# Optimization experiments

Hardware: AMD Instinct MI355X
Metric: run time of the kernel (lower is better)

Reference implementation:

```python
import jax, jax.numpy as jnp
import numpy as np
from jax import lax

H, N, L = 256, 64, 4096
DT_MIN, DT_MAX = 0.001, 0.1


def make_hippo(n_state):
    n = jnp.arange(n_state)
    P = jnp.sqrt(1.0 + 2.0 * n)
    A = P[:, None] * P[None, :]
    A = jnp.tril(A) - jnp.diag(n.astype(jnp.float32))
    B = jnp.sqrt(2.0 * n + 1.0)[:, None]
    return -A, B


def setup_inputs() -> dict:
    key = jax.random.key(0)
    A, B = make_hippo(N)
    A = jnp.broadcast_to(A, (H, N, N))            # H N N
    B = jnp.broadcast_to(B, (H, N, 1))            # H N 1
    log_dt = jnp.linspace(DT_MIN, DT_MAX, H)      # note: used directly as dt (as in source)
    u = jax.random.normal(key, (L,), dtype=jnp.float32)
    return {"u": u, "A": A, "B": B, "log_dt": log_dt}


def reference(u, A, B, log_dt):
    dt = log_dt  # `.dt` property returns log_dt.value unchanged
    I = jnp.eye(N, dtype=A.dtype)
    dt2A = (dt[:, None, None] * 0.5) * A                      # H N N
    BL = jnp.linalg.inv(I - dt2A)                             # H N N (batched inv)
    Ab = BL @ (I + dt2A)                                      # H N N
    Bb = (BL * dt[:, None, None]) @ B                         # H N 1

    # Bb * u broadcast: L H N
    Bb_u = u[:, None, None] * Bb[None, :, :, 0]

    def step(x, b_k):
        x1 = jnp.einsum('hnm,hm->hn', Ab, x) + b_k            # H N
        return x1, x1

    state0 = jnp.zeros((H, N), dtype=u.dtype)
    _, x = lax.scan(step, state0, Bb_u)                       # x: L H N
    return x
```

## Files before the change

### kernel.cpp

```cpp
#include <hip/hip_runtime.h>

#define NHEAD 256

typedef _Float16 f16x8 __attribute__((ext_vector_type(8)));
typedef float f32x4 __attribute__((ext_vector_type(4)));

__device__ __forceinline__ int mel(int r, int c) {
  return (r << 6) + ((((c >> 3) ^ r) & 7) << 3) + (c & 7);
}
__device__ __forceinline__ f16x8 ldfrag(const _Float16* M, int r, int u) {
  return *(const f16x8*)(M + (r << 6) + (((u ^ r) & 7) << 3));
}
__device__ __forceinline__ f32x4 MF(f16x8 a, f16x8 b, f32x4 c) {
  return __builtin_amdgcn_mfma_f32_16x16x32_f16(a, b, c, 0, 0, 0);
}

__device__ __forceinline__ void mmstep8(const _Float16* A, const _Float16* BT,
                                        _Float16* Dr, _Float16* Dt, int dr0,
                                        int nrb, int limit, int w, int c15,
                                        int g) {
  const int wc = w & 3;
  f16x8 b0 = ldfrag(BT, (wc << 4) + c15, g);
  f16x8 b1 = ldfrag(BT, (wc << 4) + c15, 4 + g);
  for (int ib = (w >> 2); ib < nrb; ib += 2) {
    f32x4 acc = {0.f, 0.f, 0.f, 0.f};
    f16x8 a0 = ldfrag(A, (ib << 4) + c15, g);
    f16x8 a1 = ldfrag(A, (ib << 4) + c15, 4 + g);
    acc = MF(a0, b0, acc);
    acc = MF(a1, b1, acc);
#pragma unroll
    for (int j = 0; j < 4; ++j) {
      const int lr = (ib << 4) + (g << 2) + j;
      if (lr < limit) {
        const int rr = dr0 + lr;
        const int cc = (wc << 4) + c15;
        const _Float16 v = (_Float16)acc[j];
        Dr[mel(rr, cc)] = v;
        Dt[mel(cc, rr)] = v;
      }
    }
  }
}

__global__ __launch_bounds__(512, 2) void hippo_fused(
    const float* __restrict__ u, const float* __restrict__ Ag,
    const float* __restrict__ Bv, const float* __restrict__ dtv,
    float* __restrict__ out) {
  const int h = blockIdx.x;
  const int t = threadIdx.x;
  const int w = t >> 6;
  const int lane = t & 63;
  const int c15 = lane & 15;
  const int g = lane >> 4;

  __shared__ __align__(16) _Float16 URV[4 * 4616];
  __shared__ __align__(16) _Float16 RING[4 * 4096];
  __shared__ __align__(16) char UNI[49152];
  __shared__ __align__(16) _Float16 PB23[2 * 4096];
  __shared__ float RED[8][64];
  __shared__ float KC[64];

  float* Ms = (float*)UNI;
  float* Xs = (float*)(UNI + 16384);
  float* invd = (float*)(UNI + 16384 + 17408);
  _Float16* PB0 = (_Float16*)UNI;
  _Float16* PB1 = PB0 + 4096;
  _Float16* PB4 = (_Float16*)(UNI + 16384);
  _Float16* PB5 = PB4 + 4096;
  _Float16* PB2 = PB23;
  _Float16* PB3 = PB23 + 4096;

  for (int s = 0; s < 4; ++s)
    for (int x = t; x < 4616; x += 512) {
      const int q = 4095 - x - s;
      URV[s * 4616 + x] = (q >= 0) ? (_Float16)u[q] : (_Float16)0.f;
    }
  const float dt = dtv[h];
  const float* Ah = Ag + (size_t)h * 4096;
  for (int idx = t; idx < 4096; idx += 512) {
    const int r = idx >> 6, c = idx & 63;
    const float a = Ah[idx];
    const float half_ = 0.5f * dt * a;
    const float id = (r == c) ? 1.0f : 0.0f;
    Ms[r * 64 + c] = id - half_;
    Xs[r * 68 + c] = id + half_;
  }
  if (t < 64) {
    Xs[t * 68 + 64] = dt * Bv[h * 64 + t];
    Xs[t * 68 + 65] = 0.f;
    Xs[t * 68 + 66] = 0.f;
    Xs[t * 68 + 67] = 0.f;
    invd[t] = 1.0f / (1.0f - 0.5f * dt * Ah[t * 65]);
  }
  __syncthreads();

  for (int k = 0; k < 64; k += 4) {
    if (t < 68) {
      const int c = t;
      const float x0 = Xs[k * 68 + c] * invd[k];
      const float x1 = (Xs[(k + 1) * 68 + c] - Ms[(k + 1) * 64 + k] * x0) * invd[k + 1];
      const float x2 = (Xs[(k + 2) * 68 + c] - Ms[(k + 2) * 64 + k] * x0 -
                        Ms[(k + 2) * 64 + k + 1] * x1) * invd[k + 2];
      const float x3 = (Xs[(k + 3) * 68 + c] - Ms[(k + 3) * 64 + k] * x0 -
                        Ms[(k + 3) * 64 + k + 1] * x1 -
                        Ms[(k + 3) * 64 + k + 2] * x2) * invd[k + 3];
      Xs[k * 68 + c] = x0;
      Xs[(k + 1) * 68 + c] = x1;
      Xs[(k + 2) * 68 + c] = x2;
      Xs[(k + 3) * 68 + c] = x3;
    }
    __syncthreads();
    const int nwork = (60 - k) * 17;
    for (int idx = t; idx < nwork; idx += 512) {
      const int r = k + 4 + idx / 17;
      const int cu = (idx % 17) * 4;
      float4 xr = *(float4*)&Xs[r * 68 + cu];
      const float m0 = Ms[r * 64 + k], m1 = Ms[r * 64 + k + 1];
      const float m2 = Ms[r * 64 + k + 2], m3 = Ms[r * 64 + k + 3];
      const float4 a0 = *(float4*)&Xs[k * 68 + cu];
      const float4 a1 = *(float4*)&Xs[(k + 1) * 68 + cu];
      const float4 a2 = *(float4*)&Xs[(k + 2) * 68 + cu];
      const float4 a3 = *(float4*)&Xs[(k + 3) * 68 + cu];
      xr.x -= m0 * a0.x + m1 * a1.x + m2 * a2.x + m3 * a3.x;
      xr.y -= m0 * a0.y + m1 * a1.y + m2 * a2.y + m3 * a3.y;
      xr.z -= m0 * a0.z + m1 * a1.z + m2 * a2.z + m3 * a3.z;
      xr.w -= m0 * a0.w + m1 * a1.w + m2 * a2.w + m3 * a3.w;
      *(float4*)&Xs[r * 68 + cu] = xr;
    }
    __syncthreads();
  }

  for (int idx = t; idx < 4096; idx += 512) {
    const int r = idx >> 6, cc = idx & 63;
    const _Float16 v = (_Float16)Xs[r * 68 + cc];
    PB0[mel(r, cc)] = v;
    PB1[mel(cc, r)] = v;
  }
  if (t < 64) {
    const float bb = Xs[t * 68 + 64];
    KC[t] = bb;
    PB2[mel(0, t)] = (_Float16)bb;
    PB3[mel(t, 0)] = (_Float16)bb;
  }
  __syncthreads();

  {
    const int mrow = t & 63;
    const float4* ar = (const float4*)(Xs + mrow * 68 + w * 8);
    const float4 av0 = ar[0], av1 = ar[1];
    const int jb = w * 8;
    RED[w][mrow] = av0.x * KC[jb] + av0.y * KC[jb + 1] + av0.z * KC[jb + 2] +
                   av0.w * KC[jb + 3] + av1.x * KC[jb + 4] + av1.y * KC[jb + 5] +
                   av1.z * KC[jb + 6] + av1.w * KC[jb + 7];
    __syncthreads();
    if (t < 64) {
      float s2 = 0.f;
#pragma unroll
      for (int qq = 0; qq < 8; ++qq) s2 += RED[qq][t];
      PB2[mel(1, t)] = (_Float16)s2;
      PB3[mel(t, 1)] = (_Float16)s2;
    }
    __syncthreads();
  }

  mmstep8(PB0, PB1, PB4, PB5, 0, 4, 64, w, c15, g); __syncthreads();
  mmstep8(PB2, PB4, PB2, PB3, 2, 1, 2, w, c15, g);  __syncthreads();
  mmstep8(PB4, PB5, PB0, PB1, 0, 4, 64, w, c15, g); __syncthreads();
  mmstep8(PB2, PB0, PB2, PB3, 4, 1, 4, w, c15, g);  __syncthreads();
  mmstep8(PB0, PB1, PB4, PB5, 0, 4, 64, w, c15, g); __syncthreads();
  mmstep8(PB2, PB4, PB2, PB3, 8, 1, 8, w, c15, g);  __syncthreads();
  mmstep8(PB4, PB5, PB0, PB1, 0, 4, 64, w, c15, g); __syncthreads();
  mmstep8(PB2, PB0, PB2, PB3, 16, 1, 16, w, c15, g); __syncthreads();
  mmstep8(PB0, PB1, PB4, PB5, 0, 4, 64, w, c15, g); __syncthreads();
  mmstep8(PB2, PB4, PB2, PB3, 32, 2, 32, w, c15, g); __syncthreads();
  mmstep8(PB4, PB5, PB0, PB1, 0, 4, 64, w, c15, g); __syncthreads();

  f16x8 bt[8][4];
  f16x8 bc[2][4];
  auto LB = [&](f16x8* dst, const _Float16* BT, int kk) {
#pragma unroll
    for (int nb = 0; nb < 4; ++nb)
      dst[nb] = ldfrag(BT, (nb << 4) + c15, (kk << 2) + g);
  };

  LB(bt[0], PB3, 0); LB(bt[1], PB3, 1);
  mmstep8(PB2, PB0, PB4, PB5, 0, 4, 64, w, c15, g); __syncthreads();
  LB(bt[2], PB5, 0); LB(bt[3], PB5, 1);
  mmstep8(PB4, PB0, PB2, PB3, 0, 4, 64, w, c15, g); __syncthreads();
  LB(bt[4], PB3, 0); LB(bt[5], PB3, 1);
  mmstep8(PB2, PB0, PB4, PB5, 0, 4, 64, w, c15, g); __syncthreads();
  LB(bt[6], PB5, 0); LB(bt[7], PB5, 1);
  mmstep8(PB1, PB0, PB2, PB3, 0, 4, 64, w, c15, g); __syncthreads();
  mmstep8(PB2, PB3, PB4, PB1, 0, 4, 64, w, c15, g); __syncthreads();
  LB(bc[0], PB1, 0); LB(bc[1], PB1, 1);
  __syncthreads();

  const int chain = w & 3;
  const int half = w >> 2;
  _Float16* ringw = RING + (chain << 12);
  float* outh = out + (h << 6);
  const int lanebase = (g << 3) - c15;

#pragma unroll 1
  for (int mstep = 0; mstep < 16; ++mstep) {
    const int c = chain + (mstep << 2);
    f32x4 acc[2][4];
#pragma unroll
    for (int ibl = 0; ibl < 2; ++ibl)
#pragma unroll
      for (int nb = 0; nb < 4; ++nb) acc[ibl][nb] = f32x4{0.f, 0.f, 0.f, 0.f};

#pragma unroll
    for (int ks = 0; ks < 8; ++ks) {
      const int tt = ks >> 1;
      const int base = 4095 - 64 * (c - tt) + ((ks & 1) << 5) + lanebase;
#pragma unroll
      for (int ibl = 0; ibl < 2; ++ibl) {
        const int ib = (half << 1) + ibl;
        const int m0 = base - (ib << 4);
        const int lo = m0 & 3;
        const uint2* p = (const uint2*)(URV + lo * 4616 + (m0 - lo));
        union { f16x8 hv; uint2 u2[2]; } ua;
        ua.u2[0] = p[0];
        ua.u2[1] = p[1];
#pragma unroll
        for (int nb = 0; nb < 4; ++nb)
          acc[ibl][nb] = MF(ua.hv, bt[ks][nb], acc[ibl][nb]);
      }
    }
    if (mstep > 0) {
#pragma unroll
      for (int kk = 0; kk < 2; ++kk)
#pragma unroll
        for (int ibl = 0; ibl < 2; ++ibl) {
          const int row = (((half << 1) + ibl) << 4) + c15;
          const f16x8 a = ldfrag(ringw, row, (kk << 2) + g);
#pragma unroll
          for (int nb = 0; nb < 4; ++nb)
            acc[ibl][nb] = MF(a, bc[kk][nb], acc[ibl][nb]);
        }
    }
    const int ob = c << 6;
#pragma unroll
    for (int ibl = 0; ibl < 2; ++ibl)
#pragma unroll
      for (int nb = 0; nb < 4; ++nb) {
        const int n = (nb << 4) + c15;
#pragma unroll
        for (int j = 0; j < 4; ++j) {
          const int i = (((half << 1) + ibl) << 4) + (g << 2) + j;
          const float v = acc[ibl][nb][j];
          ringw[mel(i, n)] = (_Float16)v;
          outh[(size_t)(ob + i) * 16384 + n] = v;
        }
      }
  }
}

extern "C" void kernel_launch(void* const* d_in, const int* in_sizes, int n_in,
                              void* d_out, int out_size, void* d_ws,
                              size_t ws_size, hipStream_t stream) {
  const float* u = (const float*)d_in[0];
  const float* A = (const float*)d_in[1];
  const float* B = (const float*)d_in[2];
  const float* dt = (const float*)d_in[3];
  float* out = (float*)d_out;
  hippo_fused<<<dim3(NHEAD), dim3(512), 0, stream>>>(u, A, B, dt, out);
}
```

Baseline: 72.05 us.

## Split fused kernel into matrix-prep and scan kernels with doubled block count

Splits the single fused kernel into a prep kernel, which computes the discretized power matrices and writes them as fp16 to workspace, and a main kernel that loads those fragments and runs the chunked scan. The main kernel uses two 256-thread blocks per head, each handling two of the four chains, so 512 blocks run instead of 256. The intent is to improve occupancy and CU utilization and to shrink per-block shared memory in the output-heavy phase. In exchange it adds a second launch and a global-memory round trip for the matrices, and each of the two blocks per head rebuilds the shifted u buffer.

```diff
diff --git a/kernel.cpp b/kernel.cpp
--- a/kernel.cpp
+++ b/kernel.cpp
@@ -42,10 +42,9 @@
   }
 }
 
-__global__ __launch_bounds__(512, 2) void hippo_fused(
-    const float* __restrict__ u, const float* __restrict__ Ag,
-    const float* __restrict__ Bv, const float* __restrict__ dtv,
-    float* __restrict__ out) {
+__global__ __launch_bounds__(512, 2) void hippo_prep(
+    const float* __restrict__ Ag, const float* __restrict__ Bv,
+    const float* __restrict__ dtv, _Float16* __restrict__ mats) {
   const int h = blockIdx.x;
   const int t = threadIdx.x;
   const int w = t >> 6;
@@ -53,8 +52,6 @@
   const int c15 = lane & 15;
   const int g = lane >> 4;
 
-  __shared__ __align__(16) _Float16 URV[4 * 4616];
-  __shared__ __align__(16) _Float16 RING[4 * 4096];
   __shared__ __align__(16) char UNI[49152];
   __shared__ __align__(16) _Float16 PB23[2 * 4096];
   __shared__ float RED[8][64];
@@ -69,12 +66,12 @@
   _Float16* PB5 = PB4 + 4096;
   _Float16* PB2 = PB23;
   _Float16* PB3 = PB23 + 4096;
-
-  for (int s = 0; s < 4; ++s)
-    for (int x = t; x < 4616; x += 512) {
-      const int q = 4095 - x - s;
-      URV[s * 4616 + x] = (q >= 0) ? (_Float16)u[q] : (_Float16)0.f;
-    }
+  _Float16* mh = mats + (size_t)h * 5 * 4096;
+
+  auto dump = [&](const _Float16* src, int slot) {
+    *(f16x8*)(mh + slot * 4096 + (t << 3)) = *(const f16x8*)(src + (t << 3));
+  };
+
   const float dt = dtv[h];
   const float* Ah = Ag + (size_t)h * 4096;
   for (int idx = t; idx < 4096; idx += 512) {
@@ -173,31 +170,67 @@
   mmstep8(PB2, PB0, PB2, PB3, 16, 1, 16, w, c15, g); __syncthreads();
   mmstep8(PB0, PB1, PB4, PB5, 0, 4, 64, w, c15, g); __syncthreads();
   mmstep8(PB2, PB4, PB2, PB3, 32, 2, 32, w, c15, g); __syncthreads();
+  dump(PB3, 0);
   mmstep8(PB4, PB5, PB0, PB1, 0, 4, 64, w, c15, g); __syncthreads();
-
+  mmstep8(PB2, PB0, PB4, PB5, 0, 4, 64, w, c15, g); __syncthreads();
+  dump(PB5, 1);
+  mmstep8(PB4, PB0, PB2, PB3, 0, 4, 64, w, c15, g); __syncthreads();
+  dump(PB3, 2);
+  mmstep8(PB2, PB0, PB4, PB5, 0, 4, 64, w, c15, g); __syncthreads();
+  dump(PB5, 3);
+  mmstep8(PB1, PB0, PB2, PB3, 0, 4, 64, w, c15, g); __syncthreads();
+  mmstep8(PB2, PB3, PB4, PB1, 0, 4, 64, w, c15, g); __syncthreads();
+  dump(PB1, 4);
+}
+
+__global__ __launch_bounds__(256, 2) void hippo_main(
+    const float* __restrict__ u, const _Float16* __restrict__ mats,
+    float* __restrict__ out) {
+  const int h = blockIdx.x >> 1;
+  const int pair = blockIdx.x & 1;
+  const int t = threadIdx.x;
+  const int w = t >> 6;
+  const int lane = t & 63;
+  const int c15 = lane & 15;
+  const int g = lane >> 4;
+
+  __shared__ __align__(16) _Float16 URV[4 * 4616];
+  __shared__ __align__(16) _Float16 RING[2 * 4096];
+
+  for (int s = 0; s < 4; ++s)
+    for (int x = t; x < 4616; x += 256) {
+      const int q = 4095 - x - s;
+      URV[s * 4616 + x] = (q >= 0) ? (_Float16)u[q] : (_Float16)0.f;
+    }
+
+  const _Float16* mh = mats + (size_t)h * 5 * 4096;
   f16x8 bt[8][4];
   f16x8 bc[2][4];
-  auto LB = [&](f16x8* dst, const _Float16* BT, int kk) {
-#pragma unroll
-    for (int nb = 0; nb < 4; ++nb)
-      dst[nb] = ldfrag(BT, (nb << 4) + c15, (kk << 2) + g);
-  };
-
-  LB(bt[0], PB3, 0); LB(bt[1], PB3, 1);
-  mmstep8(PB2, PB0, PB4, PB5, 0, 4, 64, w, c15, g); __syncthreads();
-  LB(bt[2], PB5, 0); LB(bt[3], PB5, 1);
-  mmstep8(PB4, PB0, PB2, PB3, 0, 4, 64, w, c15, g); __syncthreads();
-  LB(bt[4], PB3, 0); LB(bt[5], PB3, 1);
-  mmstep8(PB2, PB0, PB4, PB5, 0, 4, 64, w, c15, g); __syncthreads();
-  LB(bt[6], PB5, 0); LB(bt[7], PB5, 1);
-  mmstep8(PB1, PB0, PB2, PB3, 0, 4, 64, w, c15, g); __syncthreads();
-  mmstep8(PB2, PB3, PB4, PB1, 0, 4, 64, w, c15, g); __syncthreads();
-  LB(bc[0], PB1, 0); LB(bc[1], PB1, 1);
+#pragma unroll
+  for (int ks = 0; ks < 8; ++ks) {
+    const _Float16* mb = mh + (size_t)(ks >> 1) * 4096;
+    const int uu = ((ks & 1) << 2) + g;
+#pragma unroll
+    for (int nb = 0; nb < 4; ++nb) {
+      const int r = (nb << 4) + c15;
+      bt[ks][nb] = *(const f16x8*)(mb + (r << 6) + (((uu ^ r) & 7) << 3));
+    }
+  }
+#pragma unroll
+  for (int kk = 0; kk < 2; ++kk) {
+    const _Float16* mb = mh + (size_t)4 * 4096;
+    const int uu = (kk << 2) + g;
+#pragma unroll
+    for (int nb = 0; nb < 4; ++nb) {
+      const int r = (nb << 4) + c15;
+      bc[kk][nb] = *(const f16x8*)(mb + (r << 6) + (((uu ^ r) & 7) << 3));
+    }
+  }
   __syncthreads();
 
-  const int chain = w & 3;
-  const int half = w >> 2;
-  _Float16* ringw = RING + (chain << 12);
+  const int chain = (pair << 1) + (w >> 1);
+  const int half = w & 1;
+  _Float16* ringw = RING + ((w >> 1) << 12);
   float* outh = out + (h << 6);
   const int lanebase = (g << 3) - c15;
 
@@ -264,6 +297,9 @@
   const float* A = (const float*)d_in[1];
   const float* B = (const float*)d_in[2];
   const float* dt = (const float*)d_in[3];
+  _Float16* mats = (_Float16*)d_ws;
   float* out = (float*)d_out;
-  hippo_fused<<<dim3(NHEAD), dim3(512), 0, stream>>>(u, A, B, dt, out);
-}
+
+  hippo_prep<<<dim3(NHEAD), dim3(512), 0, stream>>>(A, B, dt, mats);
+  hippo_main<<<dim3(2 * NHEAD), dim3(256), 0, stream>>>(u, mats, out);
+}
```

Measured after the change: 87.39 us. 1.21x slower.

## Switch chunked scan to 32x32x16 MFMA with B operands read from LDS

Applied to the files above, without the earlier changes.

Rewrites the main chunk loop to use 32x32x16 MFMA tiles instead of 16x16x32, so each wave computes a 32x64 output block with two accumulators. The B fragments for the Toeplitz kernel powers and the chunk-transition matrix now stay in LDS (a new BKT buffer and PB3) and are reloaded every step, where before they were preloaded into registers. This cuts register pressure, and the ring buffer is moved into the reused UNI region. Launch bounds drop from 2 to 1 blocks per SM, trading occupancy for register room and adding more LDS traffic per step.

```diff
diff --git a/kernel.cpp b/kernel.cpp
--- a/kernel.cpp
+++ b/kernel.cpp
@@ -4,6 +4,7 @@
 
 typedef _Float16 f16x8 __attribute__((ext_vector_type(8)));
 typedef float f32x4 __attribute__((ext_vector_type(4)));
+typedef float f32x16 __attribute__((ext_vector_type(16)));
 
 __device__ __forceinline__ int mel(int r, int c) {
   return (r << 6) + ((((c >> 3) ^ r) & 7) << 3) + (c & 7);
@@ -13,6 +14,9 @@
 }
 __device__ __forceinline__ f32x4 MF(f16x8 a, f16x8 b, f32x4 c) {
   return __builtin_amdgcn_mfma_f32_16x16x32_f16(a, b, c, 0, 0, 0);
+}
+__device__ __forceinline__ f32x16 MF32(f16x8 a, f16x8 b, f32x16 c) {
+  return __builtin_amdgcn_mfma_f32_32x32x16_f16(a, b, c, 0, 0, 0);
 }
 
 __device__ __forceinline__ void mmstep8(const _Float16* A, const _Float16* BT,
@@ -42,7 +46,7 @@
   }
 }
 
-__global__ __launch_bounds__(512, 2) void hippo_fused(
+__global__ __launch_bounds__(512, 1) void hippo_fused(
     const float* __restrict__ u, const float* __restrict__ Ag,
     const float* __restrict__ Bv, const float* __restrict__ dtv,
     float* __restrict__ out) {
@@ -52,10 +56,12 @@
   const int lane = t & 63;
   const int c15 = lane & 15;
   const int g = lane >> 4;
+  const int l31 = lane & 31;
+  const int k8 = lane >> 5;
 
   __shared__ __align__(16) _Float16 URV[4 * 4616];
-  __shared__ __align__(16) _Float16 RING[4 * 4096];
   __shared__ __align__(16) char UNI[49152];
+  __shared__ __align__(16) _Float16 BKT[4 * 4096];
   __shared__ __align__(16) _Float16 PB23[2 * 4096];
   __shared__ float RED[8][64];
   __shared__ float KC[64];
@@ -140,7 +146,7 @@
     const float bb = Xs[t * 68 + 64];
     KC[t] = bb;
     PB2[mel(0, t)] = (_Float16)bb;
-    PB3[mel(t, 0)] = (_Float16)bb;
+    BKT[mel(t, 0)] = (_Float16)bb;
   }
   __syncthreads();
 
@@ -158,102 +164,79 @@
 #pragma unroll
       for (int qq = 0; qq < 8; ++qq) s2 += RED[qq][t];
       PB2[mel(1, t)] = (_Float16)s2;
-      PB3[mel(t, 1)] = (_Float16)s2;
+      BKT[mel(t, 1)] = (_Float16)s2;
     }
     __syncthreads();
   }
 
   mmstep8(PB0, PB1, PB4, PB5, 0, 4, 64, w, c15, g); __syncthreads();
-  mmstep8(PB2, PB4, PB2, PB3, 2, 1, 2, w, c15, g);  __syncthreads();
+  mmstep8(PB2, PB4, PB2, BKT, 2, 1, 2, w, c15, g);  __syncthreads();
   mmstep8(PB4, PB5, PB0, PB1, 0, 4, 64, w, c15, g); __syncthreads();
-  mmstep8(PB2, PB0, PB2, PB3, 4, 1, 4, w, c15, g);  __syncthreads();
+  mmstep8(PB2, PB0, PB2, BKT, 4, 1, 4, w, c15, g);  __syncthreads();
   mmstep8(PB0, PB1, PB4, PB5, 0, 4, 64, w, c15, g); __syncthreads();
-  mmstep8(PB2, PB4, PB2, PB3, 8, 1, 8, w, c15, g);  __syncthreads();
+  mmstep8(PB2, PB4, PB2, BKT, 8, 1, 8, w, c15, g);  __syncthreads();
   mmstep8(PB4, PB5, PB0, PB1, 0, 4, 64, w, c15, g); __syncthreads();
-  mmstep8(PB2, PB0, PB2, PB3, 16, 1, 16, w, c15, g); __syncthreads();
+  mmstep8(PB2, PB0, PB2, BKT, 16, 1, 16, w, c15, g); __syncthreads();
   mmstep8(PB0, PB1, PB4, PB5, 0, 4, 64, w, c15, g); __syncthreads();
-  mmstep8(PB2, PB4, PB2, PB3, 32, 2, 32, w, c15, g); __syncthreads();
+  mmstep8(PB2, PB4, PB2, BKT, 32, 2, 32, w, c15, g); __syncthreads();
   mmstep8(PB4, PB5, PB0, PB1, 0, 4, 64, w, c15, g); __syncthreads();
-
-  f16x8 bt[8][4];
-  f16x8 bc[2][4];
-  auto LB = [&](f16x8* dst, const _Float16* BT, int kk) {
-#pragma unroll
-    for (int nb = 0; nb < 4; ++nb)
-      dst[nb] = ldfrag(BT, (nb << 4) + c15, (kk << 2) + g);
-  };
-
-  LB(bt[0], PB3, 0); LB(bt[1], PB3, 1);
-  mmstep8(PB2, PB0, PB4, PB5, 0, 4, 64, w, c15, g); __syncthreads();
-  LB(bt[2], PB5, 0); LB(bt[3], PB5, 1);
-  mmstep8(PB4, PB0, PB2, PB3, 0, 4, 64, w, c15, g); __syncthreads();
-  LB(bt[4], PB3, 0); LB(bt[5], PB3, 1);
-  mmstep8(PB2, PB0, PB4, PB5, 0, 4, 64, w, c15, g); __syncthreads();
-  LB(bt[6], PB5, 0); LB(bt[7], PB5, 1);
-  mmstep8(PB1, PB0, PB2, PB3, 0, 4, 64, w, c15, g); __syncthreads();
-  mmstep8(PB2, PB3, PB4, PB1, 0, 4, 64, w, c15, g); __syncthreads();
-  LB(bc[0], PB1, 0); LB(bc[1], PB1, 1);
-  __syncthreads();
+  mmstep8(PB2, PB0, PB4, BKT + 4096, 0, 4, 64, w, c15, g); __syncthreads();
+  mmstep8(PB4, PB0, PB5, BKT + 2 * 4096, 0, 4, 64, w, c15, g); __syncthreads();
+  mmstep8(PB5, PB0, PB4, BKT + 3 * 4096, 0, 4, 64, w, c15, g); __syncthreads();
+  mmstep8(PB1, PB0, PB5, PB2, 0, 4, 64, w, c15, g); __syncthreads();
+  mmstep8(PB5, PB2, PB4, PB3, 0, 4, 64, w, c15, g); __syncthreads();
 
   const int chain = w & 3;
   const int half = w >> 2;
-  _Float16* ringw = RING + (chain << 12);
+  _Float16* ringw = (_Float16*)UNI + (chain << 12);
+  const _Float16* G4 = PB3;
   float* outh = out + (h << 6);
-  const int lanebase = (g << 3) - c15;
 
 #pragma unroll 1
   for (int mstep = 0; mstep < 16; ++mstep) {
     const int c = chain + (mstep << 2);
-    f32x4 acc[2][4];
-#pragma unroll
-    for (int ibl = 0; ibl < 2; ++ibl)
-#pragma unroll
-      for (int nb = 0; nb < 4; ++nb) acc[ibl][nb] = f32x4{0.f, 0.f, 0.f, 0.f};
-
-#pragma unroll
-    for (int ks = 0; ks < 8; ++ks) {
-      const int tt = ks >> 1;
-      const int base = 4095 - 64 * (c - tt) + ((ks & 1) << 5) + lanebase;
-#pragma unroll
-      for (int ibl = 0; ibl < 2; ++ibl) {
-        const int ib = (half << 1) + ibl;
-        const int m0 = base - (ib << 4);
-        const int lo = m0 & 3;
-        const uint2* p = (const uint2*)(URV + lo * 4616 + (m0 - lo));
-        union { f16x8 hv; uint2 u2[2]; } ua;
-        ua.u2[0] = p[0];
-        ua.u2[1] = p[1];
-#pragma unroll
-        for (int nb = 0; nb < 4; ++nb)
-          acc[ibl][nb] = MF(ua.hv, bt[ks][nb], acc[ibl][nb]);
+    f32x16 acc0 = {0.f}, acc1 = {0.f};
+#pragma unroll
+    for (int e = 0; e < 16; ++e) { acc0[e] = 0.f; acc1[e] = 0.f; }
+
+#pragma unroll
+    for (int ks = 0; ks < 16; ++ks) {
+      const int tt = ks >> 2;
+      const int m0 = 4095 - 64 * (c - tt) - (half << 5) - l31 +
+                     ((ks & 3) << 4) + (k8 << 3);
+      const int lo = m0 & 3;
+      const uint2* p = (const uint2*)(URV + lo * 4616 + (m0 - lo));
+      union { f16x8 hv; uint2 u2[2]; } ua;
+      ua.u2[0] = p[0];
+      ua.u2[1] = p[1];
+      const _Float16* bk = BKT + (tt << 12);
+      const int uu = ((ks & 3) << 1) + k8;
+      const f16x8 b0 = ldfrag(bk, l31, uu);
+      const f16x8 b1 = ldfrag(bk, 32 + l31, uu);
+      acc0 = MF32(ua.hv, b0, acc0);
+      acc1 = MF32(ua.hv, b1, acc1);
+    }
+    if (mstep > 0) {
+#pragma unroll
+      for (int ks = 0; ks < 4; ++ks) {
+        const int uu = (ks << 1) + k8;
+        const f16x8 a = ldfrag(ringw, (half << 5) + l31, uu);
+        const f16x8 b0 = ldfrag(G4, l31, uu);
+        const f16x8 b1 = ldfrag(G4, 32 + l31, uu);
+        acc0 = MF32(a, b0, acc0);
+        acc1 = MF32(a, b1, acc1);
       }
     }
-    if (mstep > 0) {
-#pragma unroll
-      for (int kk = 0; kk < 2; ++kk)
-#pragma unroll
-        for (int ibl = 0; ibl < 2; ++ibl) {
-          const int row = (((half << 1) + ibl) << 4) + c15;
-          const f16x8 a = ldfrag(ringw, row, (kk << 2) + g);
-#pragma unroll
-          for (int nb = 0; nb < 4; ++nb)
-            acc[ibl][nb] = MF(a, bc[kk][nb], acc[ibl][nb]);
-        }
-    }
-    const int ob = c << 6;
-#pragma unroll
-    for (int ibl = 0; ibl < 2; ++ibl)
-#pragma unroll
-      for (int nb = 0; nb < 4; ++nb) {
-        const int n = (nb << 4) + c15;
-#pragma unroll
-        for (int j = 0; j < 4; ++j) {
-          const int i = (((half << 1) + ibl) << 4) + (g << 2) + j;
-          const float v = acc[ibl][nb][j];
-          ringw[mel(i, n)] = (_Float16)v;
-          outh[(size_t)(ob + i) * 16384 + n] = v;
-        }
-      }
+    const int ob = (c << 6) + (half << 5);
+#pragma unroll
+    for (int j = 0; j < 16; ++j) {
+      const int r = (j & 3) + ((j >> 2) << 3) + (k8 << 2);
+      const float v0 = acc0[j], v1 = acc1[j];
+      ringw[mel((half << 5) + r, l31)] = (_Float16)v0;
+      ringw[mel((half << 5) + r, 32 + l31)] = (_Float16)v1;
+      outh[(size_t)(ob + r) * 16384 + l31] = v0;
+      outh[(size_t)(ob + r) * 16384 + 32 + l31] = v1;
+    }
   }
 }
 
```

After: 74.95 us. 1.04x slower.
